# Performance work log

Hardware: AMD Instinct MI355X
Metric: run time of the kernel (lower is better)

Reference implementation:

```python
import jax, jax.numpy as jnp
import numpy as np

K = 22                       # structuring element is 22x22 ones
ORIGIN = K // 2              # kornia origin = k//2 -> pad (11 before, 10 after)
PAD = ((0, 0), (0, 0), (ORIGIN, K - ORIGIN - 1), (ORIGIN, K - ORIGIN - 1))
WIN = (1, 1, K, K)
STRIDES = (1, 1, 1, 1)


def _erode(x):
    # flat (all-ones) structuring element erosion == sliding-window min.
    # Padding with +inf matches kornia's 'pad with max_val' for erosion.
    return jax.lax.reduce_window(x, float('inf'), jax.lax.min, WIN, STRIDES, PAD)


def _dilate(x):
    # flat dilation == sliding-window max; pad with -inf (kornia pads -max_val).
    return jax.lax.reduce_window(x, float('-inf'), jax.lax.max, WIN, STRIDES, PAD)


def setup_inputs() -> dict:
    key = jax.random.key(0)
    image = jax.random.uniform(key, (8, 3, 1024, 1024), dtype=jnp.float32)
    return {"image": image}


def reference(image):
    # morphological opening = erosion followed by dilation (same kernel)
    return _dilate(_erode(image))
```

## Files before the change

### kernel.cpp

```cpp
#include <hip/hip_runtime.h>


#define HH 1024
#define WW 1024
#define KW 22
#define SB 116
#define PINF __builtin_inff()

template<bool IS_MIN>
__device__ __forceinline__ float vop(float a, float b) {
    return IS_MIN ? fminf(a, b) : fmaxf(a, b);
}

template<bool IS_MIN, int CMAX, class Get, class Put>
__device__ __forceinline__ void vanherk(int cout, Get get, Put put) {
    const float ID = IS_MIN ? PINF : -PINF;
    constexpr int NB = (CMAX + 2 * KW - 2) / KW;
    float Sprev[KW];
    #pragma unroll
    for (int j = 0; j < NB; ++j) {
        const int base = KW * j;
        int needed = cout + KW - 1 - base;
        if (needed > KW) needed = KW;
        float v[KW];
        #pragma unroll
        for (int m = 0; m < KW; ++m)
            v[m] = (m < needed) ? get(base + m) : ID;
        float p = ID;
        #pragma unroll
        for (int m = 0; m < KW; ++m) {
            p = vop<IS_MIN>(p, v[m]);
            const int k = base - (KW - 1) + m;
            if (k >= 0) {
                if (m == KW - 1) {
                    if (k < cout) put(k, p);
                } else {
                    if (k < cout) put(k, vop<IS_MIN>(Sprev[m + 1], p));
                }
            }
        }
        if (j < NB - 1) {
            float s = ID;
            #pragma unroll
            for (int m = KW - 1; m >= 0; --m) {
                s = vop<IS_MIN>(s, v[m]);
                Sprev[m] = s;
            }
        }
    }
}

template<bool INTERIOR>
__device__ __forceinline__ void tile_body(const float* __restrict__ src,
                                          float* __restrict__ dst,
                                          int R, int C, float* B, int t) {
    if (t < 216) {
        const int ch = t >= 108;
        const int j = t - ch * 108;
        const int base_o = ch ? 43 : 0;
        const int cout = ch ? 42 : 43;
        int cj = C - 22 + j;
        bool colOK = true;
        if (!INTERIOR) {
            colOK = (unsigned)cj < WW;
            cj = cj < 0 ? 0 : (cj > WW - 1 ? WW - 1 : cj);
        }
        const float* col = src + cj;
        const int rbase = R - 22 + base_o;
        vanherk<true, 43>(cout,
            [&](int p) {
                int r = rbase + p;
                if (INTERIOR) return col[r * WW];
                int rc = r < 0 ? 0 : (r > HH - 1 ? HH - 1 : r);
                float v = col[rc * WW];
                return (colOK && (unsigned)r < HH) ? v : PINF;
            },
            [&](int k, float v) { B[(base_o + k) * SB + j] = v; });
    }
    __syncthreads();

    {
        float res[44];
        const bool act = t < 170;
        int o = 0, e0 = 0;
        if (act) {
            o = t >> 1;
            const int ch = t & 1;
            e0 = ch ? 44 : 0;
            const int cout = ch ? 41 : 44;
            const int n = cout + KW - 1;
            float in[68];
            const float4* Br = (const float4*)(B + o * SB + e0);
            #pragma unroll
            for (int i = 0; i < 17; ++i) {
                if (4 * i < n) {
                    float4 x = Br[i];
                    in[4 * i] = x.x; in[4 * i + 1] = x.y;
                    in[4 * i + 2] = x.z; in[4 * i + 3] = x.w;
                }
            }
            vanherk<true, 44>(cout,
                [&](int p) { return in[p]; },
                [&](int k, float v) { res[k] = v; });
            if (!INTERIOR) {
                const bool rOK = (unsigned)(R - 11 + o) < HH;
                #pragma unroll
                for (int k = 0; k < 44; ++k) {
                    const int cimg = C - 11 + e0 + k;
                    if (!rOK || (unsigned)cimg >= WW) res[k] = -PINF;
                }
            }
        }
        __syncthreads();
        if (act) {
            float4* Bw = (float4*)(B + o * SB + e0);
            #pragma unroll
            for (int i = 0; i < 11; ++i)
                Bw[i] = make_float4(res[4 * i], res[4 * i + 1],
                                    res[4 * i + 2], res[4 * i + 3]);
        }
        __syncthreads();
    }

    {
        float res[32];
        const bool act = t < 170;
        int o = 0, c0 = 0;
        if (act) {
            o = t >> 1;
            c0 = (t & 1) * 32;
            float in[56];
            const float4* Br = (const float4*)(B + o * SB + c0);
            #pragma unroll
            for (int i = 0; i < 14; ++i) {
                float4 x = Br[i];
                in[4 * i] = x.x; in[4 * i + 1] = x.y;
                in[4 * i + 2] = x.z; in[4 * i + 3] = x.w;
            }
            vanherk<false, 32>(32,
                [&](int p) { return in[p]; },
                [&](int k, float v) { res[k] = v; });
        }
        __syncthreads();
        if (act) {
            float4* Bw = (float4*)(B + o * SB + c0);
            #pragma unroll
            for (int i = 0; i < 8; ++i)
                Bw[i] = make_float4(res[4 * i], res[4 * i + 1],
                                    res[4 * i + 2], res[4 * i + 3]);
        }
        __syncthreads();
    }

    if (t < 128) {
        const int c = t & 63;
        const int y0 = (t >> 6) << 5;
        float o32[32];
        vanherk<false, 32>(32,
            [&](int p) { return B[(y0 + p) * SB + c]; },
            [&](int k, float v) { o32[k] = v; });
        #pragma unroll
        for (int k = 0; k < 32; ++k)
            dst[(R + y0 + k) * WW + C + c] = o32[k];
    }
}

__global__ __launch_bounds__(256) void fused_open(const float* __restrict__ in,
                                                  float* __restrict__ out) {
    __shared__ float B[85 * SB];
    const int t = threadIdx.x;
    const int b = blockIdx.x;
    const int plane = b >> 8;
    const int by = (b >> 4) & 15;
    const int bx = b & 15;
    const int R = by * 64, C = bx * 64;
    const float* src = in + (size_t)plane * (HH * WW);
    float* dst = out + (size_t)plane * (HH * WW);

    if (by >= 1 && by <= 14 && bx >= 1 && bx <= 14)
        tile_body<true>(src, dst, R, C, B, t);
    else
        tile_body<false>(src, dst, R, C, B, t);
}

extern "C" void kernel_launch(void* const* d_in, const int* in_sizes, int n_in,
                              void* d_out, int out_size, void* d_ws, size_t ws_size,
                              hipStream_t stream) {
    const float* in = (const float*)d_in[0];
    float* out = (float*)d_out;
    (void)d_ws; (void)ws_size;
    fused_open<<<24 * 16 * 16, 256, 0, stream>>>(in, out);
}
```

Before: 188.1 us.

## Fuse horizontal erode/dilate passes per row and drop intermediate block barriers

```diff
diff --git a/kernel.cpp b/kernel.cpp
--- a/kernel.cpp
+++ b/kernel.cpp
@@ -12,30 +12,29 @@
     return IS_MIN ? fminf(a, b) : fmaxf(a, b);
 }
 
-template<bool IS_MIN, int CMAX, class Get, class Put>
-__device__ __forceinline__ void vanherk(int cout, Get get, Put put) {
+template<bool IS_MIN, int COUT, class Get, class Put>
+__device__ __forceinline__ void vanherk(Get get, Put put) {
+    constexpr int NIN = COUT + KW - 1;
+    constexpr int NB = (NIN + KW - 1) / KW;
     const float ID = IS_MIN ? PINF : -PINF;
-    constexpr int NB = (CMAX + 2 * KW - 2) / KW;
     float Sprev[KW];
     #pragma unroll
     for (int j = 0; j < NB; ++j) {
         const int base = KW * j;
-        int needed = cout + KW - 1 - base;
-        if (needed > KW) needed = KW;
+        const int needed = (NIN - base) < KW ? (NIN - base) : KW;
         float v[KW];
         #pragma unroll
         for (int m = 0; m < KW; ++m)
-            v[m] = (m < needed) ? get(base + m) : ID;
+            if (m < needed) v[m] = get(base + m);
         float p = ID;
         #pragma unroll
         for (int m = 0; m < KW; ++m) {
-            p = vop<IS_MIN>(p, v[m]);
-            const int k = base - (KW - 1) + m;
-            if (k >= 0) {
-                if (m == KW - 1) {
-                    if (k < cout) put(k, p);
-                } else {
-                    if (k < cout) put(k, vop<IS_MIN>(Sprev[m + 1], p));
+            if (m < needed) {
+                p = vop<IS_MIN>(p, v[m]);
+                const int k = base - (KW - 1) + m;
+                if (k >= 0 && k < COUT) {
+                    if (m == KW - 1) put(k, p);
+                    else             put(k, vop<IS_MIN>(Sprev[m + 1], p));
                 }
             }
         }
@@ -56,9 +55,8 @@
                                           int R, int C, float* B, int t) {
     if (t < 216) {
         const int ch = t >= 108;
-        const int j = t - ch * 108;
+        const int j = ch ? t - 108 : t;
         const int base_o = ch ? 43 : 0;
-        const int cout = ch ? 42 : 43;
         int cj = C - 22 + j;
         bool colOK = true;
         if (!INTERIOR) {
@@ -67,107 +65,99 @@
         }
         const float* col = src + cj;
         const int rbase = R - 22 + base_o;
-        vanherk<true, 43>(cout,
+        vanherk<true, 43>(
             [&](int p) {
                 int r = rbase + p;
                 if (INTERIOR) return col[r * WW];
                 int rc = r < 0 ? 0 : (r > HH - 1 ? HH - 1 : r);
-                float v = col[rc * WW];
-                return (colOK && (unsigned)r < HH) ? v : PINF;
+                float vv = col[rc * WW];
+                return (colOK && (unsigned)r < HH) ? vv : PINF;
             },
-            [&](int k, float v) { B[(base_o + k) * SB + j] = v; });
+            [&](int k, float vv) { B[(base_o + k) * SB + j] = vv; });
     }
     __syncthreads();
 
-    {
-        float res[44];
-        const bool act = t < 170;
-        int o = 0, e0 = 0;
-        if (act) {
-            o = t >> 1;
-            const int ch = t & 1;
-            e0 = ch ? 44 : 0;
-            const int cout = ch ? 41 : 44;
-            const int n = cout + KW - 1;
-            float in[68];
-            const float4* Br = (const float4*)(B + o * SB + e0);
+    if (t < 170) {
+        const int o = t >> 1;
+        const int half = t & 1;
+        float* Brow = B + o * SB;
+
+        const int e0 = half * 44;
+        float in1[68];
+        {
+            const float4* Br = (const float4*)(Brow + e0);
             #pragma unroll
             for (int i = 0; i < 17; ++i) {
-                if (4 * i < n) {
-                    float4 x = Br[i];
-                    in[4 * i] = x.x; in[4 * i + 1] = x.y;
-                    in[4 * i + 2] = x.z; in[4 * i + 3] = x.w;
-                }
-            }
-            vanherk<true, 44>(cout,
-                [&](int p) { return in[p]; },
-                [&](int k, float v) { res[k] = v; });
-            if (!INTERIOR) {
-                const bool rOK = (unsigned)(R - 11 + o) < HH;
-                #pragma unroll
-                for (int k = 0; k < 44; ++k) {
-                    const int cimg = C - 11 + e0 + k;
-                    if (!rOK || (unsigned)cimg >= WW) res[k] = -PINF;
-                }
+                float4 x = Br[i];
+                in1[4 * i] = x.x; in1[4 * i + 1] = x.y;
+                in1[4 * i + 2] = x.z; in1[4 * i + 3] = x.w;
             }
         }
-        __syncthreads();
-        if (act) {
-            float4* Bw = (float4*)(B + o * SB + e0);
+        float er[44];
+        vanherk<true, 44>(
+            [&](int p) { return in1[p]; },
+            [&](int k, float vv) { er[k] = vv; });
+        if (!INTERIOR) {
+            const bool rOK = (unsigned)(R - 11 + o) < HH;
+            #pragma unroll
+            for (int k = 0; k < 44; ++k) {
+                const int cimg = C - 11 + e0 + k;
+                if (!rOK || (unsigned)cimg >= WW) er[k] = -PINF;
+            }
+        }
+        __threadfence_block();
+        {
+            float4* Bw = (float4*)(Brow + e0);
             #pragma unroll
             for (int i = 0; i < 11; ++i)
-                Bw[i] = make_float4(res[4 * i], res[4 * i + 1],
-                                    res[4 * i + 2], res[4 * i + 3]);
+                Bw[i] = make_float4(er[4 * i], er[4 * i + 1],
+                                    er[4 * i + 2], er[4 * i + 3]);
         }
-        __syncthreads();
-    }
+        __threadfence_block();
 
-    {
-        float res[32];
-        const bool act = t < 170;
-        int o = 0, c0 = 0;
-        if (act) {
-            o = t >> 1;
-            c0 = (t & 1) * 32;
-            float in[56];
-            const float4* Br = (const float4*)(B + o * SB + c0);
+        const int c0 = half * 32;
+        float in2[56];
+        {
+            const float4* Br = (const float4*)(Brow + c0);
             #pragma unroll
             for (int i = 0; i < 14; ++i) {
                 float4 x = Br[i];
-                in[4 * i] = x.x; in[4 * i + 1] = x.y;
-                in[4 * i + 2] = x.z; in[4 * i + 3] = x.w;
+                in2[4 * i] = x.x; in2[4 * i + 1] = x.y;
+                in2[4 * i + 2] = x.z; in2[4 * i + 3] = x.w;
             }
-            vanherk<false, 32>(32,
-                [&](int p) { return in[p]; },
-                [&](int k, float v) { res[k] = v; });
         }
-        __syncthreads();
-        if (act) {
-            float4* Bw = (float4*)(B + o * SB + c0);
+        float rx[32];
+        vanherk<false, 32>(
+            [&](int p) { return in2[p]; },
+            [&](int k, float vv) { rx[k] = vv; });
+        __threadfence_block();
+        {
+            float4* Bw = (float4*)(Brow + c0);
             #pragma unroll
             for (int i = 0; i < 8; ++i)
-                Bw[i] = make_float4(res[4 * i], res[4 * i + 1],
-                                    res[4 * i + 2], res[4 * i + 3]);
+                Bw[i] = make_float4(rx[4 * i], rx[4 * i + 1],
+                                    rx[4 * i + 2], rx[4 * i + 3]);
         }
-        __syncthreads();
     }
+    __syncthreads();
 
-    if (t < 128) {
-        const int c = t & 63;
-        const int y0 = (t >> 6) << 5;
+    if (t >= 128) {
+        const int tt = t - 128;
+        const int c = tt & 63;
+        const int y0 = (tt >> 6) << 5;
         float o32[32];
-        vanherk<false, 32>(32,
+        vanherk<false, 32>(
             [&](int p) { return B[(y0 + p) * SB + c]; },
-            [&](int k, float v) { o32[k] = v; });
+            [&](int k, float vv) { o32[k] = vv; });
         #pragma unroll
         for (int k = 0; k < 32; ++k)
             dst[(R + y0 + k) * WW + C + c] = o32[k];
     }
 }
 
-__global__ __launch_bounds__(256) void fused_open(const float* __restrict__ in,
-                                                  float* __restrict__ out) {
-    __shared__ float B[85 * SB];
+__global__ __launch_bounds__(256, 4) void fused_open(const float* __restrict__ in,
+                                                     float* __restrict__ out) {
+    __shared__ float B[86 * SB];
     const int t = threadIdx.x;
     const int b = blockIdx.x;
     const int plane = b >> 8;
```

Result: no change. 187.2 us (-0.5%).
